# Optimization experiments

Measured on AMD Instinct MI355X. Metric: run time of the kernel, lower is better.

The kernel has to match this reference:

```python
import jax, jax.numpy as jnp
import numpy as np

B, S, D, M, E, K = 2, 2048, 1024, 1408, 8, 2  # batch, seq, n_embed, n_moe_mlp, n_experts, top_k


def setup_inputs() -> dict:
    key = jax.random.key(0)
    k0, k1, k2, k3, k4 = jax.random.split(key, 5)
    scale = 0.02
    return {
        "x": jax.random.normal(k0, (B, S, D), dtype=jnp.float32),
        "w_gate": jax.random.normal(k1, (D, E), dtype=jnp.float32) * scale,  # gate.weight.T
        "w_g": jax.random.normal(k2, (E, D, M), dtype=jnp.float32) * scale,  # gate_proj.weight.T per expert
        "w_u": jax.random.normal(k3, (E, D, M), dtype=jnp.float32) * scale,  # up_proj.weight.T per expert
        "w_d": jax.random.normal(k4, (E, M, D), dtype=jnp.float32) * scale,  # down_proj.weight.T per expert
    }


def reference(x, w_gate, w_g, w_u, w_d):
    # router
    scores = x @ w_gate                                  # [B,S,E]
    topk_scores, topk_idx = jax.lax.top_k(scores, K)     # [B,S,K]
    topk_probs = jax.nn.softmax(topk_scores, axis=-1)    # softmax over selected experts only
    # scatter top-k probs back to dense [B,S,E] gating (top_k indices are distinct)
    gating = jnp.sum(
        jax.nn.one_hot(topk_idx, E, dtype=topk_probs.dtype) * topk_probs[..., None],
        axis=-2,
    )                                                    # [B,S,E]
    # dense all-expert SwiGLU (faithful to the compute-then-mask original)
    hidden = jax.nn.silu(jnp.einsum("bsd,edm->ebsm", x, w_g)) * jnp.einsum(
        "bsd,edm->ebsm", x, w_u
    )                                                    # [E,B,S,M]
    expert_out = jnp.einsum("ebsm,emd->ebsd", hidden, w_d)  # [E,B,S,D]
    # masked weighted combine
    y = jnp.einsum("bse,ebsd->bsd", gating, expert_out)  # [B,S,D]
    return y
```

## Files before the change

### kernel.cpp

```cpp
#include <hip/hip_runtime.h>
#include <cstdio>

constexpr int T  = 4096;
constexpr int D  = 1024;
constexpr int M  = 1408;
constexpr int E  = 8;

constexpr int TM = 128;
constexpr int TN = 128;
constexpr int BK = 32;
constexpr int RCAP = T * 2 + E * TM;
constexpr int MT_MAX = T / TM;
constexpr int NT_UP = M / TN;
constexpr int NT_DN = D / TN;

constexpr int CSTR = 64;
constexpr int TOKB = 16;
constexpr int RTB  = T / TOKB;
constexpr int XCV  = (T * D) / 2048;
constexpr int TP_PER_W = E * 2816 / 8;
constexpr int PREP_GRID = RTB + XCV + 3 * TP_PER_W;

typedef _Float16 half8 __attribute__((ext_vector_type(8)));
typedef _Float16 half4 __attribute__((ext_vector_type(4)));
typedef float    floatx4 __attribute__((ext_vector_type(4)));

#define VMW12() asm volatile("s_waitcnt vmcnt(12)" ::: "memory")
#define VMW8()  asm volatile("s_waitcnt vmcnt(8)"  ::: "memory")
#define VMW6()  asm volatile("s_waitcnt vmcnt(6)"  ::: "memory")
#define VMW4()  asm volatile("s_waitcnt vmcnt(4)"  ::: "memory")
#define VMW0()  asm volatile("s_waitcnt vmcnt(0)"  ::: "memory")

constexpr size_t OFF_COUNTS = 0;
constexpr size_t OFF_BASE   = (size_t)E * CSTR * 4;
constexpr size_t OFF_PC     = OFF_BASE + 64;
constexpr size_t OFF_TOTAL  = OFF_PC + 64;
constexpr size_t OFF_T2E    = OFF_TOTAL + 64;
constexpr size_t OFF_T2POS  = OFF_T2E   + (size_t)2 * T * 4;
constexpr size_t OFF_T2P    = OFF_T2POS + (size_t)2 * T * 4;
constexpr size_t OFF_TLIST  = OFF_T2P   + (size_t)2 * T * 4;
constexpr size_t OFF_XG     = OFF_TLIST + (size_t)E * T * 4;
constexpr size_t OFF_HID    = OFF_XG  + (size_t)RCAP * D * 2;
constexpr size_t OFF_WGT    = OFF_HID + (size_t)RCAP * M * 2;
constexpr size_t OFF_WUT    = OFF_WGT + (size_t)E * M * D * 2;
constexpr size_t OFF_WDT    = OFF_WUT + (size_t)E * M * D * 2;
constexpr size_t WS_NEED    = OFF_WDT + (size_t)E * D * M * 2;

__device__ __forceinline__ void gl_lds16(const void* g, void* l) {
  __builtin_amdgcn_global_load_lds(
      (const __attribute__((address_space(1))) unsigned int*)g,
      (__attribute__((address_space(3))) unsigned int*)l, 16, 0, 0);
}

__device__ __forceinline__ void expert_base_pc(const int* __restrict__ counts,
                                               int e, int& base_e, int& pc_e,
                                               int& cnt_e) {
  int b = 0; base_e = 0; pc_e = 0; cnt_e = 0;
  #pragma unroll
  for (int ee = 0; ee < E; ++ee) {
    int c = counts[ee * CSTR];
    int p = (c + TM - 1) / TM * TM;
    if (ee == e) { base_e = b; pc_e = p; cnt_e = c; }
    b += p;
  }
}

__global__ __launch_bounds__(256) void k_prep(
    const float* __restrict__ x, const float* __restrict__ wgate,
    const float* __restrict__ w_g, const float* __restrict__ w_u,
    const float* __restrict__ w_d,
    _Float16* __restrict__ Xh,
    _Float16* __restrict__ wgT, _Float16* __restrict__ wuT, _Float16* __restrict__ wdT,
    int* __restrict__ counts, int* __restrict__ tlist,
    int* __restrict__ t2e, int* __restrict__ t2pos, float* __restrict__ t2p) {
  __shared__ float tile[4][32][33];
  __shared__ int   s_cnt[E];
  __shared__ int   s_base[E];
  __shared__ int   s_e[2 * TOKB];
  __shared__ int   s_pos[2 * TOKB];
  __shared__ float s_p[2 * TOKB];
  int bid = blockIdx.x;

  if (bid < RTB) {
    int wv = threadIdx.x >> 6, lane = threadIdx.x & 63;
    if (threadIdx.x < E) s_cnt[threadIdx.x] = 0;
    __syncthreads();
    for (int j = 0; j < TOKB / 4; ++j) {
      int tl = wv * (TOKB / 4) + j;
      int t  = bid * TOKB + tl;
      const float* xr = x + (size_t)t * D;
      float acc[E] = {0.f,0.f,0.f,0.f,0.f,0.f,0.f,0.f};
      #pragma unroll
      for (int i = 0; i < D / 64; ++i) {
        int d = i * 64 + lane;
        float xv = xr[d];
        const float4* wr2 = (const float4*)(wgate + (size_t)d * E);
        float4 w0 = wr2[0], w1 = wr2[1];
        acc[0] += xv * w0.x; acc[1] += xv * w0.y; acc[2] += xv * w0.z; acc[3] += xv * w0.w;
        acc[4] += xv * w1.x; acc[5] += xv * w1.y; acc[6] += xv * w1.z; acc[7] += xv * w1.w;
      }
      #pragma unroll
      for (int e = 0; e < E; ++e) {
        #pragma unroll
        for (int off = 32; off; off >>= 1) acc[e] += __shfl_xor(acc[e], off, 64);
      }
      if (lane == 0) {
        int i0 = 0; float s0 = acc[0];
        #pragma unroll
        for (int e = 1; e < E; ++e) if (acc[e] > s0) { s0 = acc[e]; i0 = e; }
        int i1 = -1; float s1 = -1e30f;
        #pragma unroll
        for (int e = 0; e < E; ++e) if (e != i0 && acc[e] > s1) { s1 = acc[e]; i1 = e; }
        float p0 = 1.f / (1.f + expf(s1 - s0));
        float p1 = 1.f - p0;
        int q0 = atomicAdd(&s_cnt[i0], 1);
        int q1 = atomicAdd(&s_cnt[i1], 1);
        s_e[2 * tl]     = i0; s_pos[2 * tl]     = q0; s_p[2 * tl]     = p0;
        s_e[2 * tl + 1] = i1; s_pos[2 * tl + 1] = q1; s_p[2 * tl + 1] = p1;
      }
    }
    __syncthreads();
    if (threadIdx.x < E)
      s_base[threadIdx.x] = atomicAdd(&counts[threadIdx.x * CSTR], s_cnt[threadIdx.x]);
    __syncthreads();
    if (threadIdx.x < 2 * TOKB) {
      int sl = threadIdx.x;
      int e = s_e[sl];
      int pos = s_base[e] + s_pos[sl];
      int t = bid * TOKB + (sl >> 1);
      tlist[e * T + pos] = t;
      t2e[2 * t + (sl & 1)]   = e;
      t2pos[2 * t + (sl & 1)] = pos;
      t2p[2 * t + (sl & 1)]   = s_p[sl];
    }
    return;
  }

  if (bid < RTB + XCV) {
    size_t base = (size_t)(bid - RTB) * 2048 + threadIdx.x * 8;
    float4 v0 = *(const float4*)(x + base);
    float4 v1 = *(const float4*)(x + base + 4);
    half8 h;
    h[0] = (_Float16)v0.x; h[1] = (_Float16)v0.y;
    h[2] = (_Float16)v0.z; h[3] = (_Float16)v0.w;
    h[4] = (_Float16)v1.x; h[5] = (_Float16)v1.y;
    h[6] = (_Float16)v1.z; h[7] = (_Float16)v1.w;
    *(half8*)(Xh + base) = h;
    return;
  }

  int i = bid - RTB - XCV;
  int which = i / TP_PER_W;
  int j = i - which * TP_PER_W;
  const float* src; _Float16* dst; int Rr, Cc;
  if (which == 0)      { src = w_g; dst = wgT; Rr = D; Cc = M; }
  else if (which == 1) { src = w_u; dst = wuT; Rr = D; Cc = M; }
  else                 { src = w_d; dst = wdT; Rr = M; Cc = D; }
  int ctn = Cc / 128, rtn = Rr / 32;
  int e   = j / (ctn * rtn);
  int rem = j - e * (ctn * rtn);
  int rt = rem / ctn, ct = rem - rt * ctn;
  int tr  = threadIdx.x >> 3;
  int tc4 = (threadIdx.x & 7) * 4;
  const float* s = src + ((size_t)e * Rr + rt * 32 + tr) * Cc + ct * 128 + tc4;
  float4 v[4];
  #pragma unroll
  for (int q = 0; q < 4; ++q) v[q] = *(const float4*)(s + q * 32);
  #pragma unroll
  for (int q = 0; q < 4; ++q) {
    tile[q][tr][tc4 + 0] = v[q].x; tile[q][tr][tc4 + 1] = v[q].y;
    tile[q][tr][tc4 + 2] = v[q].z; tile[q][tr][tc4 + 3] = v[q].w;
  }
  __syncthreads();
  #pragma unroll
  for (int q = 0; q < 4; ++q) {
    union { _Float16 h[4]; ushort4 u; } o;
    #pragma unroll
    for (int p = 0; p < 4; ++p) o.h[p] = (_Float16)tile[q][tc4 + p][tr];
    *(ushort4*)(dst + ((size_t)e * Cc + ct * 128 + q * 32 + tr) * Rr + rt * 32 + tc4) = o.u;
  }
}

__global__ __launch_bounds__(256, 2) void k_upgate(
    const _Float16* __restrict__ Xh, const _Float16* __restrict__ wgT,
    const _Float16* __restrict__ wuT, _Float16* __restrict__ Hid,
    const int* __restrict__ counts, const int* __restrict__ tlist) {
  int lin = blockIdx.x;
  int e = lin & 7;
  int r = lin >> 3;
  int nt = r % NT_UP;
  int mt = r / NT_UP;
  int base_e, pc_e, cnt_e;
  expert_base_pc(counts, e, base_e, pc_e, cnt_e);
  if (mt * TM >= pc_e) return;
  int row0 = base_e + mt * TM;
  int n0 = nt * TN;
  __shared__ _Float16 As[3][TM * BK];
  __shared__ _Float16 Bg[3][TN * BK];
  __shared__ _Float16 Bu[3][TN * BK];
  int tid = threadIdx.x;
  int w = tid >> 6, lane = tid & 63;
  int lrow = lane & 15, quad = lane >> 4;
  int wr = w >> 1, wc = w & 1;
  int sr = lane >> 2;
  int c4 = lane & 3;
  int swc = ((c4 ^ ((sr >> 1) & 3))) * 8;

  const _Float16* wg_e = wgT + (size_t)e * M * D;
  const _Float16* wu_e = wuT + (size_t)e * M * D;
  const _Float16* pA[2]; const _Float16* pG[2]; const _Float16* pU[2];
  int loff[2];
  #pragma unroll
  for (int is = 0; is < 2; ++is) {
    int grow = w * 32 + is * 16 + sr;
    int local = mt * TM + grow;
    int trow = (local < cnt_e) ? tlist[e * T + local] : 0;
    pA[is] = Xh   + (size_t)trow * D + swc;
    pG[is] = wg_e + (size_t)(n0 + grow) * D + swc;
    pU[is] = wu_e + (size_t)(n0 + grow) * D + swc;
    loff[is] = (w * 2 + is) * 1024;
  }

  int swr = (lrow >> 1) & 3;

  floatx4 accg[4][4] = {};
  floatx4 accu[4][4] = {};

  auto stage = [&](int b) {
    char* a0 = (char*)&As[b][0];
    char* g0 = (char*)&Bg[b][0];
    char* u0 = (char*)&Bu[b][0];
    #pragma unroll
    for (int is = 0; is < 2; ++is) {
      gl_lds16(pA[is], a0 + loff[is]); pA[is] += BK;
      gl_lds16(pG[is], g0 + loff[is]); pG[is] += BK;
      gl_lds16(pU[is], u0 + loff[is]); pU[is] += BK;
    }
  };
  auto compute = [&](int b) {
    int kc = (quad ^ swr) * 8;
    half8 af[4];
    #pragma unroll
    for (int i = 0; i < 4; ++i)
      af[i] = *(const half8*)&As[b][(wr * 64 + i * 16 + lrow) * BK + kc];
    #pragma unroll
    for (int c = 0; c < 4; ++c) {
      int bo = (wc * 64 + c * 16 + lrow) * BK + kc;
      half8 bgc = *(const half8*)&Bg[b][bo];
      half8 buc = *(const half8*)&Bu[b][bo];
      #pragma unroll
      for (int i = 0; i < 4; ++i) {
        accg[c][i] = __builtin_amdgcn_mfma_f32_16x16x32_f16(af[i], bgc, accg[c][i], 0, 0, 0);
        accu[c][i] = __builtin_amdgcn_mfma_f32_16x16x32_f16(af[i], buc, accu[c][i], 0, 0, 0);
      }
    }
  };

  constexpr int NTK = D / BK;
  stage(0); stage(1);
  for (int k = 0; k < NTK; ++k) {
    if (k + 2 < NTK) {
      stage((k + 2) % 3);
      VMW12();
    } else if (k + 1 < NTK) {
      VMW6();
    } else {
      VMW0();
    }
    __builtin_amdgcn_sched_barrier(0);
    __builtin_amdgcn_s_barrier();
    compute(k % 3);
    __builtin_amdgcn_s_barrier();
  }

  #pragma unroll
  for (int c = 0; c < 4; ++c) {
    int col = n0 + wc * 64 + c * 16 + lrow;
    #pragma unroll
    for (int i = 0; i < 4; ++i) {
      int rowb = row0 + wr * 64 + i * 16 + quad * 4;
      #pragma unroll
      for (int reg = 0; reg < 4; ++reg) {
        float g = accg[c][i][reg], u = accu[c][i][reg];
        Hid[(size_t)(rowb + reg) * M + col] = (_Float16)(g / (1.f + expf(-g)) * u);
      }
    }
  }
}

__global__ __launch_bounds__(256, 2) void k_down(
    const _Float16* __restrict__ Hid, const _Float16* __restrict__ wdT,
    _Float16* __restrict__ Yp, const int* __restrict__ counts) {
  int lin = blockIdx.x;
  int e = lin & 7;
  int r = lin >> 3;
  int nt = r % NT_DN;
  int mt = r / NT_DN;
  int base_e, pc_e, cnt_e;
  expert_base_pc(counts, e, base_e, pc_e, cnt_e);
  if (mt * TM >= pc_e) return;
  int row0 = base_e + mt * TM;
  int d0 = nt * TN;
  __shared__ _Float16 As[3][TM * BK];
  __shared__ _Float16 Bs[3][TN * BK];
  int tid = threadIdx.x;
  int w = tid >> 6, lane = tid & 63;
  int lrow = lane & 15, quad = lane >> 4;
  int wr = w >> 1, wc = w & 1;
  int sr = lane >> 2;
  int c4 = lane & 3;
  int swc = ((c4 ^ ((sr >> 1) & 3))) * 8;

  const _Float16* wd_e = wdT + (size_t)e * D * M;
  const _Float16* pA[2]; const _Float16* pB[2];
  int loff[2];
  #pragma unroll
  for (int is = 0; is < 2; ++is) {
    int grow = w * 32 + is * 16 + sr;
    pA[is] = Hid  + (size_t)(row0 + grow) * M + swc;
    pB[is] = wd_e + (size_t)(d0   + grow) * M + swc;
    loff[is] = (w * 2 + is) * 1024;
  }

  int swr = (lrow >> 1) & 3;

  floatx4 acc[4][4] = {};

  auto stage = [&](int b) {
    char* a0 = (char*)&As[b][0];
    char* b0 = (char*)&Bs[b][0];
    #pragma unroll
    for (int is = 0; is < 2; ++is) {
      gl_lds16(pA[is], a0 + loff[is]); pA[is] += BK;
      gl_lds16(pB[is], b0 + loff[is]); pB[is] += BK;
    }
  };
  auto compute = [&](int b) {
    int kc = (quad ^ swr) * 8;
    half8 af[4];
    #pragma unroll
    for (int i = 0; i < 4; ++i)
      af[i] = *(const half8*)&As[b][(wr * 64 + i * 16 + lrow) * BK + kc];
    #pragma unroll
    for (int c = 0; c < 4; ++c) {
      half8 bc = *(const half8*)&Bs[b][(wc * 64 + c * 16 + lrow) * BK + kc];
      #pragma unroll
      for (int i = 0; i < 4; ++i)
        acc[c][i] = __builtin_amdgcn_mfma_f32_16x16x32_f16(af[i], bc, acc[c][i], 0, 0, 0);
    }
  };

  constexpr int NTK = M / BK;
  stage(0); stage(1);
  for (int k = 0; k < NTK; ++k) {
    if (k + 2 < NTK) {
      stage((k + 2) % 3);
      VMW8();
    } else if (k + 1 < NTK) {
      VMW4();
    } else {
      VMW0();
    }
    __builtin_amdgcn_sched_barrier(0);
    __builtin_amdgcn_s_barrier();
    compute(k % 3);
    __builtin_amdgcn_s_barrier();
  }

  #pragma unroll
  for (int c = 0; c < 4; ++c) {
    int col = d0 + wc * 64 + c * 16 + lrow;
    #pragma unroll
    for (int i = 0; i < 4; ++i) {
      int rowb = row0 + wr * 64 + i * 16 + quad * 4;
      #pragma unroll
      for (int reg = 0; reg < 4; ++reg)
        Yp[(size_t)(rowb + reg) * D + col] = (_Float16)acc[c][i][reg];
    }
  }
}

__global__ __launch_bounds__(256) void k_combine(
    const _Float16* __restrict__ Yp, const int* __restrict__ counts,
    const int* __restrict__ t2e, const int* __restrict__ t2pos,
    const float* __restrict__ t2p, float* __restrict__ out) {
  int t = blockIdx.x;
  int e0 = t2e[2 * t], e1 = t2e[2 * t + 1];
  int b = 0, b0 = 0, b1 = 0;
  #pragma unroll
  for (int ee = 0; ee < E; ++ee) {
    if (ee == e0) b0 = b;
    if (ee == e1) b1 = b;
    int c = counts[ee * CSTR];
    b += (c + TM - 1) / TM * TM;
  }
  int r0 = b0 + t2pos[2 * t];
  int r1 = b1 + t2pos[2 * t + 1];
  float p0 = t2p[2 * t], p1 = t2p[2 * t + 1];
  int d = threadIdx.x * 4;
  half4 h0 = *(const half4*)(Yp + (size_t)r0 * D + d);
  half4 h1 = *(const half4*)(Yp + (size_t)r1 * D + d);
  float4 o;
  o.x = p0 * (float)h0.x + p1 * (float)h1.x;
  o.y = p0 * (float)h0.y + p1 * (float)h1.y;
  o.z = p0 * (float)h0.z + p1 * (float)h1.z;
  o.w = p0 * (float)h0.w + p1 * (float)h1.w;
  *(float4*)(out + (size_t)t * D + d) = o;
}

extern "C" void kernel_launch(void* const* d_in, const int* in_sizes, int n_in,
                              void* d_out, int out_size, void* d_ws, size_t ws_size,
                              hipStream_t stream) {
  const float* x     = (const float*)d_in[0];
  const float* wgate = (const float*)d_in[1];
  const float* w_g   = (const float*)d_in[2];
  const float* w_u   = (const float*)d_in[3];
  const float* w_d   = (const float*)d_in[4];
  float* out = (float*)d_out;
  char* ws = (char*)d_ws;

  if (ws_size < WS_NEED) {
    fprintf(stderr, "kernel_launch: ws_size=%zu < needed %zu\n", ws_size, WS_NEED);
    return;
  }

  int* counts = (int*)(ws + OFF_COUNTS);
  int* t2e    = (int*)(ws + OFF_T2E);
  int* t2pos  = (int*)(ws + OFF_T2POS);
  float* t2p  = (float*)(ws + OFF_T2P);
  int* tlist  = (int*)(ws + OFF_TLIST);
  _Float16* Xh  = (_Float16*)(ws + OFF_XG);
  _Float16* Hid = (_Float16*)(ws + OFF_HID);
  _Float16* wgT = (_Float16*)(ws + OFF_WGT);
  _Float16* wuT = (_Float16*)(ws + OFF_WUT);
  _Float16* wdT = (_Float16*)(ws + OFF_WDT);

  hipMemsetAsync(counts, 0, (size_t)E * CSTR * 4, stream);

  k_prep<<<PREP_GRID, 256, 0, stream>>>(x, wgate, w_g, w_u, w_d, Xh,
                                        wgT, wuT, wdT,
                                        counts, tlist, t2e, t2pos, t2p);
  k_upgate<<<E * MT_MAX * NT_UP, 256, 0, stream>>>(Xh, wgT, wuT, Hid, counts, tlist);
  _Float16* Yp = Xh;
  k_down<<<E * MT_MAX * NT_DN, 256, 0, stream>>>(Hid, wdT, Yp, counts);
  k_combine<<<T, 256, 0, stream>>>(Yp, counts, t2e, t2pos, t2p, out);
}
```

Baseline: 297.8 us.

## Move down-proj weight transpose into upgate kernel and widen transpose tiles

The fp32-to-fp16 transpose of w_d is moved out of the prep kernel and appended as extra blocks in the up/gate GEMM launch, so it can overlap with GEMM work rather than sitting on the critical path before it. The transpose itself changes to 64x64 tiles with 16-byte half8 stores instead of 32x128 tiles with 8-byte stores. The trade-off is that the GEMM grid gains extra transpose blocks that compete for CUs, and the GEMM shared memory is reused as the transpose tile.

```diff
diff --git a/kernel.cpp b/kernel.cpp
--- a/kernel.cpp
+++ b/kernel.cpp
@@ -18,8 +18,10 @@
 constexpr int TOKB = 16;
 constexpr int RTB  = T / TOKB;
 constexpr int XCV  = (T * D) / 2048;
-constexpr int TP_PER_W = E * 2816 / 8;
-constexpr int PREP_GRID = RTB + XCV + 3 * TP_PER_W;
+constexpr int TPW  = E * (D / 64) * (M / 64);
+constexpr int PREP_GRID = RTB + XCV + 2 * TPW;
+constexpr int NGEMM_UP  = E * MT_MAX * NT_UP;
+constexpr int UPG_GRID  = NGEMM_UP + TPW;
 
 typedef _Float16 half8 __attribute__((ext_vector_type(8)));
 typedef _Float16 half4 __attribute__((ext_vector_type(4)));
@@ -65,15 +67,47 @@
   }
 }
 
+__device__ __forceinline__ void transpose64(
+    const float* __restrict__ src, _Float16* __restrict__ dst,
+    int Rr, int Cc, int j, float (*tile)[69]) {
+  int ctn = Cc >> 6, rtn = Rr >> 6;
+  int e   = j / (ctn * rtn);
+  int rem = j - e * (ctn * rtn);
+  int rt = rem / ctn, ct = rem - rt * ctn;
+  int t = threadIdx.x;
+  int lr = t >> 2;
+  int lc = (t & 3) * 16;
+  const float* s = src + ((size_t)e * Rr + rt * 64 + lr) * Cc + ct * 64 + lc;
+  float4 v0 = *(const float4*)(s + 0);
+  float4 v1 = *(const float4*)(s + 4);
+  float4 v2 = *(const float4*)(s + 8);
+  float4 v3 = *(const float4*)(s + 12);
+  float* tr = &tile[lr][lc];
+  tr[0]  = v0.x; tr[1]  = v0.y; tr[2]  = v0.z; tr[3]  = v0.w;
+  tr[4]  = v1.x; tr[5]  = v1.y; tr[6]  = v1.z; tr[7]  = v1.w;
+  tr[8]  = v2.x; tr[9]  = v2.y; tr[10] = v2.z; tr[11] = v2.w;
+  tr[12] = v3.x; tr[13] = v3.y; tr[14] = v3.z; tr[15] = v3.w;
+  __syncthreads();
+  #pragma unroll
+  for (int rep = 0; rep < 2; ++rep) {
+    int s2 = t + rep * 256;
+    int oc = s2 >> 3;
+    int sl = s2 & 7;
+    half8 o;
+    #pragma unroll
+    for (int q = 0; q < 8; ++q) o[q] = (_Float16)tile[sl * 8 + q][oc];
+    *(half8*)(dst + ((size_t)e * Cc + ct * 64 + oc) * Rr + rt * 64 + sl * 8) = o;
+  }
+}
+
 __global__ __launch_bounds__(256) void k_prep(
     const float* __restrict__ x, const float* __restrict__ wgate,
     const float* __restrict__ w_g, const float* __restrict__ w_u,
-    const float* __restrict__ w_d,
     _Float16* __restrict__ Xh,
-    _Float16* __restrict__ wgT, _Float16* __restrict__ wuT, _Float16* __restrict__ wdT,
+    _Float16* __restrict__ wgT, _Float16* __restrict__ wuT,
     int* __restrict__ counts, int* __restrict__ tlist,
     int* __restrict__ t2e, int* __restrict__ t2pos, float* __restrict__ t2p) {
-  __shared__ float tile[4][32][33];
+  __shared__ float tile[64][69];
   __shared__ int   s_cnt[E];
   __shared__ int   s_base[E];
   __shared__ int   s_e[2 * TOKB];
@@ -150,42 +184,24 @@
   }
 
   int i = bid - RTB - XCV;
-  int which = i / TP_PER_W;
-  int j = i - which * TP_PER_W;
-  const float* src; _Float16* dst; int Rr, Cc;
-  if (which == 0)      { src = w_g; dst = wgT; Rr = D; Cc = M; }
-  else if (which == 1) { src = w_u; dst = wuT; Rr = D; Cc = M; }
-  else                 { src = w_d; dst = wdT; Rr = M; Cc = D; }
-  int ctn = Cc / 128, rtn = Rr / 32;
-  int e   = j / (ctn * rtn);
-  int rem = j - e * (ctn * rtn);
-  int rt = rem / ctn, ct = rem - rt * ctn;
-  int tr  = threadIdx.x >> 3;
-  int tc4 = (threadIdx.x & 7) * 4;
-  const float* s = src + ((size_t)e * Rr + rt * 32 + tr) * Cc + ct * 128 + tc4;
-  float4 v[4];
-  #pragma unroll
-  for (int q = 0; q < 4; ++q) v[q] = *(const float4*)(s + q * 32);
-  #pragma unroll
-  for (int q = 0; q < 4; ++q) {
-    tile[q][tr][tc4 + 0] = v[q].x; tile[q][tr][tc4 + 1] = v[q].y;
-    tile[q][tr][tc4 + 2] = v[q].z; tile[q][tr][tc4 + 3] = v[q].w;
-  }
-  __syncthreads();
-  #pragma unroll
-  for (int q = 0; q < 4; ++q) {
-    union { _Float16 h[4]; ushort4 u; } o;
-    #pragma unroll
-    for (int p = 0; p < 4; ++p) o.h[p] = (_Float16)tile[q][tc4 + p][tr];
-    *(ushort4*)(dst + ((size_t)e * Cc + ct * 128 + q * 32 + tr) * Rr + rt * 32 + tc4) = o.u;
-  }
+  if (i < TPW) transpose64(w_g, wgT, D, M, i, tile);
+  else         transpose64(w_u, wuT, D, M, i - TPW, tile);
 }
 
 __global__ __launch_bounds__(256, 2) void k_upgate(
     const _Float16* __restrict__ Xh, const _Float16* __restrict__ wgT,
     const _Float16* __restrict__ wuT, _Float16* __restrict__ Hid,
-    const int* __restrict__ counts, const int* __restrict__ tlist) {
+    const int* __restrict__ counts, const int* __restrict__ tlist,
+    const float* __restrict__ w_d, _Float16* __restrict__ wdT) {
+  __shared__ _Float16 As[3][TM * BK];
+  __shared__ _Float16 Bg[3][TN * BK];
+  __shared__ _Float16 Bu[3][TN * BK];
   int lin = blockIdx.x;
+  if (lin >= NGEMM_UP) {
+    float (*tile)[69] = reinterpret_cast<float (*)[69]>(&As[0][0]);
+    transpose64(w_d, wdT, M, D, lin - NGEMM_UP, tile);
+    return;
+  }
   int e = lin & 7;
   int r = lin >> 3;
   int nt = r % NT_UP;
@@ -195,9 +211,6 @@
   if (mt * TM >= pc_e) return;
   int row0 = base_e + mt * TM;
   int n0 = nt * TN;
-  __shared__ _Float16 As[3][TM * BK];
-  __shared__ _Float16 Bg[3][TN * BK];
-  __shared__ _Float16 Bu[3][TN * BK];
   int tid = threadIdx.x;
   int w = tid >> 6, lane = tid & 63;
   int lrow = lane & 15, quad = lane >> 4;
@@ -437,10 +450,11 @@
 
   hipMemsetAsync(counts, 0, (size_t)E * CSTR * 4, stream);
 
-  k_prep<<<PREP_GRID, 256, 0, stream>>>(x, wgate, w_g, w_u, w_d, Xh,
-                                        wgT, wuT, wdT,
+  k_prep<<<PREP_GRID, 256, 0, stream>>>(x, wgate, w_g, w_u, Xh,
+                                        wgT, wuT,
                                         counts, tlist, t2e, t2pos, t2p);
-  k_upgate<<<E * MT_MAX * NT_UP, 256, 0, stream>>>(Xh, wgT, wuT, Hid, counts, tlist);
+  k_upgate<<<UPG_GRID, 256, 0, stream>>>(Xh, wgT, wuT, Hid, counts, tlist,
+                                         w_d, wdT);
   _Float16* Yp = Xh;
   k_down<<<E * MT_MAX * NT_DN, 256, 0, stream>>>(Hid, wdT, Yp, counts);
   k_combine<<<T, 256, 0, stream>>>(Yp, counts, t2e, t2pos, t2p, out);
```

New measurement: 288.5 us. 1.03x faster.
